# Performance work log

Hardware: AMD Instinct MI355X
Metric: run time of the kernel (lower is better)

The kernel has to match this reference:

```python
import jax, jax.numpy as jnp
import numpy as np

DT = 0.01
REG = 0.01

def setup_inputs() -> dict:
    key = jax.random.key(0)
    k1, k2, k3, k4 = jax.random.split(key, 4)
    B, C_in, L = 16, 128, 4096
    C_out, KS = 256, 9
    return {
        "x": jax.random.normal(k1, (B, C_in, L), dtype=jnp.float32),
        "weight": jax.random.normal(k2, (C_out, C_in, KS), dtype=jnp.float32) * np.sqrt(2.0 / (C_out * KS)),
        "bias": jnp.zeros((C_out,), dtype=jnp.float32),
        "vel": jax.random.normal(k3, (C_in, KS), dtype=jnp.float32) * 0.1,
        "acc": jax.random.normal(k4, (C_in, KS), dtype=jnp.float32) * 0.01,
        "ks": 9,
        "stride": 1,
        "pad": 4,
    }

def reference(x, weight, bias, vel, acc, ks, stride, pad):
    # x: [B, C_in, L]
    if pad > 0:
        x = jnp.pad(x, ((0, 0), (0, 0), (pad, pad)), mode="edge")  # replicate pad
    L_pad = x.shape[2]
    L_out = (L_pad - ks) // stride + 1
    t_off = jnp.arange(ks, dtype=jnp.float32) * DT  # [ks]
    # unfold: gather sliding windows -> [B, C_in, L_out, ks]
    idx = jnp.arange(L_out)[:, None] * stride + jnp.arange(ks)[None, :]
    xu = x[:, :, idx]
    # per-tap physics offset: vel*t + 0.5*acc*t^2, shape [C_in, ks] broadcast
    offset = vel * t_off + 0.5 * acc * (t_off ** 2)  # [C_in, ks]
    xt = xu + offset[None, :, None, :]  # [B, C_in, L_out, ks]
    # GEMM: [B, L_out, C_in*ks] x [C_in*ks, C_out]
    out = jnp.einsum("bclk,ock->bol", xt, weight) + bias[None, :, None]
    phys = REG * (jnp.mean(vel ** 2) + jnp.mean(acc ** 2))
    return (out, phys)
```

## Files before the change

### kernel.cpp

```cpp
#include <hip/hip_runtime.h>
#include <hip/hip_bf16.h>

typedef unsigned short u16;
typedef __bf16 bf16x8 __attribute__((ext_vector_type(8)));
typedef float f32x4 __attribute__((ext_vector_type(4)));
typedef unsigned short ushort8 __attribute__((ext_vector_type(8)));

#define C_IN   128
#define C_OUT  256
#define BATCH  16
#define LEN    4096
#define KS     9
#define PAD    4
#define LPAD   (LEN + 2*PAD)
#define KTOT   (C_IN * KS)
#define NSTEP  36

#define XT_BLKS    1040
#define W4_BLKS    1152
#define EB_BLKS    256

__device__ inline u16 f2bf(float f) {
    __hip_bfloat16 h = __float2bfloat16(f);
    return __builtin_bit_cast(u16, h);
}

__device__ __forceinline__ void g2l16(const void* g, void* l) {
    __builtin_amdgcn_global_load_lds(
        (const __attribute__((address_space(1))) void*)g,
        (__attribute__((address_space(3))) void*)l, 16, 0, 0);
}

__global__ void prep_all(const float* __restrict__ x, const float* __restrict__ w,
                         const float* __restrict__ bias, const float* __restrict__ vel,
                         const float* __restrict__ acc_in,
                         u16* __restrict__ xt, u16* __restrict__ w4,
                         float* __restrict__ ebias, float* __restrict__ phys_out) {
    int bid = blockIdx.x;
    int t = threadIdx.x;
    if (bid < XT_BLKS) {
        int b    = bid / 65;
        int lblk = bid % 65;
        int lane = t & 63;
        int jb   = t >> 6;
        int lp   = lblk * 64 + lane;
        if (lp >= LPAD) return;
        int l = lp - PAD;
        l = l < 0 ? 0 : (l > LEN - 1 ? LEN - 1 : l);
        const float* xb = x + (size_t)b * C_IN * LEN + l;
        u16* row = xt + ((size_t)b * LPAD + lp) * C_IN;
        int key = lp & 15;
        #pragma unroll
        for (int jj = 0; jj < 4; ++jj) {
            int cblk = jb * 4 + jj;
            ushort8 v;
            #pragma unroll
            for (int e = 0; e < 8; ++e)
                v[e] = f2bf(xb[(size_t)(cblk * 8 + e) * LEN]);
            int jstore = cblk ^ key;
            *reinterpret_cast<ushort8*>(row + jstore * 8) = v;
        }
        return;
    }
    if (bid < XT_BLKS + W4_BLKS) {
        int i = (bid - XT_BLKS) * 256 + t;
        int e  = i & 7;
        int r  = i >> 3;
        int mr = r & 15;
        int kg = (r >> 4) & 3;
        int ob = (r >> 6) & 15;
        int s  = r >> 10;
        int o  = ob * 16 + mr;
        int k  = s >> 2;
        int c  = (s & 3) * 32 + kg * 8 + e;
        w4[i] = f2bf(w[((size_t)o * C_IN + c) * KS + k]);
        return;
    }
    __shared__ float red[256];
    int o = bid - (XT_BLKS + W4_BLKS);
    float sum = 0.f;
    for (int i = t; i < KTOT; i += 256) {
        int k = i % KS;
        float tk = k * 0.01f;
        float off = vel[i] * tk + 0.5f * acc_in[i] * tk * tk;
        sum += off * w[(size_t)o * KTOT + i];
    }
    red[t] = sum;
    __syncthreads();
    for (int h = 128; h > 0; h >>= 1) {
        if (t < h) red[t] += red[t + h];
        __syncthreads();
    }
    if (t == 0) ebias[o] = bias[o] + red[0];

    if (o == 0) {
        __syncthreads();
        float pv = 0.f;
        for (int i = t; i < KTOT; i += 256) {
            float v = vel[i], a = acc_in[i];
            pv += v * v + a * a;
        }
        red[t] = pv;
        __syncthreads();
        for (int h = 128; h > 0; h >>= 1) {
            if (t < h) red[t] += red[t + h];
            __syncthreads();
        }
        if (t == 0) *phys_out = 0.01f * (red[0] / (float)KTOT);
    }
}

__global__ __launch_bounds__(256, 2) void conv_main(const u16* __restrict__ xt,
                                                    const u16* __restrict__ w4,
                                                    const float* __restrict__ ebias,
                                                    float* __restrict__ out) {
    __shared__ u16 ldsx[17408];
    __shared__ u16 ldsa[2][8192];

    int b     = blockIdx.y;
    int lbase = blockIdx.x * 128;
    int t     = threadIdx.x;
    int lane  = t & 63;
    int w     = t >> 6;
    int wm    = w >> 1;
    int wn    = w & 1;
    int mrow  = lane & 15;
    int kgrp  = lane >> 4;

    {
        const u16* bsrc = xt + ((size_t)b * LPAD + lbase) * C_IN;
        #pragma unroll
        for (int j = 0; j < 8; ++j)
            g2l16(bsrc + (j * 256 + t) * 8, ldsx + (j * 256 + w * 64) * 8);
        if (t < 128)
            g2l16(bsrc + (2048 + t) * 8, ldsx + (2048 + w * 64) * 8);
        #pragma unroll
        for (int j = 0; j < 4; ++j)
            g2l16(w4 + (j * 256 + t) * 8, ldsa[0] + (j * 256 + w * 64) * 8);
    }
    __syncthreads();

    f32x4 acc[8][4] = {};
    const char* ldsbase = reinterpret_cast<const char*>(ldsx);
    int afoff = (wm << 13) + lane * 16;

    #define LOAD_A_BUF(BUF, AF)                                                  \
        {                                                                        \
            const char* ab_ = reinterpret_cast<const char*>(ldsa[BUF]) + afoff;  \
            _Pragma("unroll")                                                    \
            for (int mi = 0; mi < 8; ++mi)                                       \
                AF[mi] = *reinterpret_cast<const bf16x8*>(ab_ + (mi << 10));     \
        }
    #define LOAD_B(S, BF)                                                        \
        {                                                                        \
            int k_ = (S) >> 2;                                                   \
            int coff_ = ((S) & 3) * 64 + kgrp * 16;                              \
            _Pragma("unroll")                                                    \
            for (int ni = 0; ni < 4; ++ni) {                                     \
                int row_  = wn * 64 + ni * 16 + mrow + k_;                       \
                int addr_ = row_ * 256 + coff_;                                  \
                addr_ ^= (row_ & 15) << 4;                                       \
                BF[ni] = *reinterpret_cast<const bf16x8*>(ldsbase + addr_);      \
            }                                                                    \
        }
    #define STAGE_A(S, BUF)                                                      \
        {                                                                        \
            const u16* as_ = w4 + (size_t)(S) * 8192;                            \
            _Pragma("unroll")                                                    \
            for (int j = 0; j < 4; ++j)                                          \
                g2l16(as_ + (j * 256 + t) * 8, ldsa[BUF] + (j * 256 + w * 64) * 8); \
        }

    #pragma unroll
    for (int s = 0; s < NSTEP; ++s) {
        if (s + 1 < NSTEP) STAGE_A(s + 1, (s + 1) & 1);
        bf16x8 af[8], bf[4];
        LOAD_A_BUF(s & 1, af);
        LOAD_B(s, bf);
        #pragma unroll
        for (int mi = 0; mi < 8; ++mi)
            #pragma unroll
            for (int ni = 0; ni < 4; ++ni)
                acc[mi][ni] = __builtin_amdgcn_mfma_f32_16x16x32_bf16(
                    af[mi], bf[ni], acc[mi][ni], 0, 0, 0);
        if (s + 1 < NSTEP) {
            asm volatile("s_waitcnt vmcnt(0) lgkmcnt(0)" ::: "memory");
            __builtin_amdgcn_s_barrier();
        }
    }

    #pragma unroll
    for (int mi = 0; mi < 8; ++mi) {
        int o0 = wm * 128 + mi * 16 + kgrp * 4;
        f32x4 eb = *reinterpret_cast<const f32x4*>(ebias + o0);
        #pragma unroll
        for (int ni = 0; ni < 4; ++ni) {
            int l = lbase + wn * 64 + ni * 16 + mrow;
            float* op = out + (size_t)(b * C_OUT + o0) * LEN + l;
            #pragma unroll
            for (int r = 0; r < 4; ++r)
                op[(size_t)r * LEN] = acc[mi][ni][r] + eb[r];
        }
    }
    #undef LOAD_A_BUF
    #undef LOAD_B
    #undef STAGE_A
}

extern "C" void kernel_launch(void* const* d_in, const int* in_sizes, int n_in,
                              void* d_out, int out_size, void* d_ws, size_t ws_size,
                              hipStream_t stream) {
    const float* x      = (const float*)d_in[0];
    const float* weight = (const float*)d_in[1];
    const float* bias   = (const float*)d_in[2];
    const float* vel    = (const float*)d_in[3];
    const float* acc    = (const float*)d_in[4];
    float* out = (float*)d_out;

    char* ws = (char*)d_ws;
    u16*  xt    = (u16*)ws;
    u16*  w4    = (u16*)(ws + (size_t)BATCH * LPAD * C_IN * 2);
    float* ebias = (float*)(ws + (size_t)BATCH * LPAD * C_IN * 2 + (size_t)C_OUT * KTOT * 2);

    hipLaunchKernelGGL(prep_all, dim3(XT_BLKS + W4_BLKS + EB_BLKS), dim3(256), 0, stream,
                       x, weight, bias, vel, acc, xt, w4, ebias,
                       out + (size_t)BATCH * C_OUT * LEN);
    hipLaunchKernelGGL(conv_main, dim3(LEN / 128, BATCH), dim3(256), 0, stream,
                       xt, w4, ebias, out);
}
```

Measured before the change: 58.57 us.

## Load weight fragments directly from global into registers, drop LDS staging and barriers

The weight operand is no longer staged through double-buffered LDS with a block-wide barrier every step. Each wave now reads its own 64-row slice of weights straight from global memory into registers, with register double-buffering across steps. The warp tiling changes from a 2x2 grid to 4x1, so each wave covers all 128 positions and reads more B fragments from LDS. This removes per-step synchronisation and LDS traffic for A, at the cost of direct global latency being exposed and less A reuse across waves.

```diff
diff --git a/kernel.cpp b/kernel.cpp
--- a/kernel.cpp
+++ b/kernel.cpp
@@ -115,15 +115,13 @@
                                                     const float* __restrict__ ebias,
                                                     float* __restrict__ out) {
     __shared__ u16 ldsx[17408];
-    __shared__ u16 ldsa[2][8192];
 
     int b     = blockIdx.y;
     int lbase = blockIdx.x * 128;
     int t     = threadIdx.x;
     int lane  = t & 63;
     int w     = t >> 6;
-    int wm    = w >> 1;
-    int wn    = w & 1;
+    int wm    = w;
     int mrow  = lane & 15;
     int kgrp  = lane >> 4;
 
@@ -134,77 +132,66 @@
             g2l16(bsrc + (j * 256 + t) * 8, ldsx + (j * 256 + w * 64) * 8);
         if (t < 128)
             g2l16(bsrc + (2048 + t) * 8, ldsx + (2048 + w * 64) * 8);
-        #pragma unroll
-        for (int j = 0; j < 4; ++j)
-            g2l16(w4 + (j * 256 + t) * 8, ldsa[0] + (j * 256 + w * 64) * 8);
     }
     __syncthreads();
 
-    f32x4 acc[8][4] = {};
+    f32x4 acc[4][8] = {};
     const char* ldsbase = reinterpret_cast<const char*>(ldsx);
-    int afoff = (wm << 13) + lane * 16;
-
-    #define LOAD_A_BUF(BUF, AF)                                                  \
+    const u16* alane = w4 + ((size_t)(wm * 4) * 64 + lane) * 8;
+
+    #define LOAD_A(S, AF)                                                        \
         {                                                                        \
-            const char* ab_ = reinterpret_cast<const char*>(ldsa[BUF]) + afoff;  \
+            const u16* p_ = alane + (size_t)(S) * 8192;                          \
             _Pragma("unroll")                                                    \
-            for (int mi = 0; mi < 8; ++mi)                                       \
-                AF[mi] = *reinterpret_cast<const bf16x8*>(ab_ + (mi << 10));     \
-        }
-    #define LOAD_B(S, BF)                                                        \
+            for (int mi = 0; mi < 4; ++mi)                                       \
+                AF[mi] = *reinterpret_cast<const bf16x8*>(p_ + mi * 512);        \
+        }
+    #define STEP(S, AF)                                                          \
         {                                                                        \
             int k_ = (S) >> 2;                                                   \
             int coff_ = ((S) & 3) * 64 + kgrp * 16;                              \
+            bf16x8 bf_[8];                                                       \
             _Pragma("unroll")                                                    \
-            for (int ni = 0; ni < 4; ++ni) {                                     \
-                int row_  = wn * 64 + ni * 16 + mrow + k_;                       \
+            for (int ni = 0; ni < 8; ++ni) {                                     \
+                int row_  = ni * 16 + mrow + k_;                                 \
                 int addr_ = row_ * 256 + coff_;                                  \
                 addr_ ^= (row_ & 15) << 4;                                       \
-                BF[ni] = *reinterpret_cast<const bf16x8*>(ldsbase + addr_);      \
+                bf_[ni] = *reinterpret_cast<const bf16x8*>(ldsbase + addr_);     \
             }                                                                    \
-        }
-    #define STAGE_A(S, BUF)                                                      \
-        {                                                                        \
-            const u16* as_ = w4 + (size_t)(S) * 8192;                            \
             _Pragma("unroll")                                                    \
-            for (int j = 0; j < 4; ++j)                                          \
-                g2l16(as_ + (j * 256 + t) * 8, ldsa[BUF] + (j * 256 + w * 64) * 8); \
-        }
+            for (int mi = 0; mi < 4; ++mi)                                       \
+                _Pragma("unroll")                                                \
+                for (int ni = 0; ni < 8; ++ni)                                   \
+                    acc[mi][ni] = __builtin_amdgcn_mfma_f32_16x16x32_bf16(       \
+                        AF[mi], bf_[ni], acc[mi][ni], 0, 0, 0);                  \
+        }
+
+    bf16x8 afA[4], afB[4];
+    LOAD_A(0, afA);
 
     #pragma unroll
-    for (int s = 0; s < NSTEP; ++s) {
-        if (s + 1 < NSTEP) STAGE_A(s + 1, (s + 1) & 1);
-        bf16x8 af[8], bf[4];
-        LOAD_A_BUF(s & 1, af);
-        LOAD_B(s, bf);
-        #pragma unroll
-        for (int mi = 0; mi < 8; ++mi)
-            #pragma unroll
-            for (int ni = 0; ni < 4; ++ni)
-                acc[mi][ni] = __builtin_amdgcn_mfma_f32_16x16x32_bf16(
-                    af[mi], bf[ni], acc[mi][ni], 0, 0, 0);
-        if (s + 1 < NSTEP) {
-            asm volatile("s_waitcnt vmcnt(0) lgkmcnt(0)" ::: "memory");
-            __builtin_amdgcn_s_barrier();
-        }
+    for (int s = 0; s < NSTEP; s += 2) {
+        if (s + 1 < NSTEP) LOAD_A(s + 1, afB);
+        STEP(s, afA);
+        if (s + 2 < NSTEP) LOAD_A(s + 2, afA);
+        STEP(s + 1, afB);
     }
 
     #pragma unroll
-    for (int mi = 0; mi < 8; ++mi) {
-        int o0 = wm * 128 + mi * 16 + kgrp * 4;
+    for (int mi = 0; mi < 4; ++mi) {
+        int o0 = wm * 64 + mi * 16 + kgrp * 4;
         f32x4 eb = *reinterpret_cast<const f32x4*>(ebias + o0);
         #pragma unroll
-        for (int ni = 0; ni < 4; ++ni) {
-            int l = lbase + wn * 64 + ni * 16 + mrow;
+        for (int ni = 0; ni < 8; ++ni) {
+            int l = lbase + ni * 16 + mrow;
             float* op = out + (size_t)(b * C_OUT + o0) * LEN + l;
             #pragma unroll
             for (int r = 0; r < 4; ++r)
                 op[(size_t)r * LEN] = acc[mi][ni][r] + eb[r];
         }
     }
-    #undef LOAD_A_BUF
-    #undef LOAD_B
-    #undef STAGE_A
+    #undef LOAD_A
+    #undef STEP
 }
 
 extern "C" void kernel_launch(void* const* d_in, const int* in_sizes, int n_in,
```

After: 71.83 us. +22.6%, slower.

## Enlarge conv tile to 512 threads with triple-buffered weight pipeline and split MFMA phases

Applied to the files above, without the earlier changes.

Doubles the per-block L tile to 256 with 8 waves arranged 2x4, so each weight stage in LDS is shared by more output columns. Weight staging moves from double to triple buffering with a prefetch distance of two, and partial vmcnt waits replace full drains. Each step is split into two half-MFMA phases with interleaved LDS loads, barriers and s_setprio. The aim is to hide global-to-LDS latency and raise weight reuse. In exchange, LDS per block grows (about 115 KB), which may cut occupancy, and the grid halves to 256 blocks.

```diff
diff --git a/kernel.cpp b/kernel.cpp
--- a/kernel.cpp
+++ b/kernel.cpp
@@ -110,20 +110,20 @@
     }
 }
 
-__global__ __launch_bounds__(256, 2) void conv_main(const u16* __restrict__ xt,
+__global__ __launch_bounds__(512, 2) void conv_main(const u16* __restrict__ xt,
                                                     const u16* __restrict__ w4,
                                                     const float* __restrict__ ebias,
                                                     float* __restrict__ out) {
-    __shared__ u16 ldsx[17408];
-    __shared__ u16 ldsa[2][8192];
+    __shared__ u16 ldsx[4224 * 8];
+    __shared__ u16 ldsa[3][8192];
 
     int b     = blockIdx.y;
-    int lbase = blockIdx.x * 128;
+    int lbase = blockIdx.x * 256;
     int t     = threadIdx.x;
     int lane  = t & 63;
     int w     = t >> 6;
-    int wm    = w >> 1;
-    int wn    = w & 1;
+    int wm    = w >> 2;
+    int wn    = w & 3;
     int mrow  = lane & 15;
     int kgrp  = lane >> 4;
 
@@ -131,27 +131,30 @@
         const u16* bsrc = xt + ((size_t)b * LPAD + lbase) * C_IN;
         #pragma unroll
         for (int j = 0; j < 8; ++j)
-            g2l16(bsrc + (j * 256 + t) * 8, ldsx + (j * 256 + w * 64) * 8);
+            g2l16(bsrc + (j * 512 + t) * 8, ldsx + (j * 512 + w * 64) * 8);
         if (t < 128)
-            g2l16(bsrc + (2048 + t) * 8, ldsx + (2048 + w * 64) * 8);
-        #pragma unroll
-        for (int j = 0; j < 4; ++j)
-            g2l16(w4 + (j * 256 + t) * 8, ldsa[0] + (j * 256 + w * 64) * 8);
-    }
-    __syncthreads();
+            g2l16(bsrc + (4096 + t) * 8, ldsx + (4096 + w * 64) * 8);
+        #pragma unroll
+        for (int p = 0; p < 2; ++p)
+            #pragma unroll
+            for (int j = 0; j < 2; ++j)
+                g2l16(w4 + (size_t)p * 8192 + (j * 512 + t) * 8,
+                      ldsa[p] + (j * 512 + w * 64) * 8);
+    }
+    asm volatile("s_waitcnt vmcnt(2)" ::: "memory");
+    __builtin_amdgcn_s_barrier();
 
     f32x4 acc[8][4] = {};
     const char* ldsbase = reinterpret_cast<const char*>(ldsx);
-    int afoff = (wm << 13) + lane * 16;
-
-    #define LOAD_A_BUF(BUF, AF)                                                  \
+
+    #define LOAD_A4(BUF, M0, AF)                                                 \
         {                                                                        \
-            const char* ab_ = reinterpret_cast<const char*>(ldsa[BUF]) + afoff;  \
+            const u16* ab_ = ldsa[BUF] + wm * 4096 + (M0) * 512 + lane * 8;      \
             _Pragma("unroll")                                                    \
-            for (int mi = 0; mi < 8; ++mi)                                       \
-                AF[mi] = *reinterpret_cast<const bf16x8*>(ab_ + (mi << 10));     \
-        }
-    #define LOAD_B(S, BF)                                                        \
+            for (int mi = 0; mi < 4; ++mi)                                       \
+                AF[mi] = *reinterpret_cast<const bf16x8*>(ab_ + mi * 512);       \
+        }
+    #define LOAD_B4(S, BF)                                                       \
         {                                                                        \
             int k_ = (S) >> 2;                                                   \
             int coff_ = ((S) & 3) * 64 + kgrp * 16;                              \
@@ -163,35 +166,49 @@
                 BF[ni] = *reinterpret_cast<const bf16x8*>(ldsbase + addr_);      \
             }                                                                    \
         }
-    #define STAGE_A(S, BUF)                                                      \
+    #define STAGE_J(S, J)                                                        \
+        g2l16(w4 + (size_t)(S) * 8192 + ((J) * 512 + t) * 8,                     \
+              ldsa[(S) % 3] + ((J) * 512 + w * 64) * 8);
+    #define MFMA16(AF, BF, M0)                                                   \
         {                                                                        \
-            const u16* as_ = w4 + (size_t)(S) * 8192;                            \
             _Pragma("unroll")                                                    \
-            for (int j = 0; j < 4; ++j)                                          \
-                g2l16(as_ + (j * 256 + t) * 8, ldsa[BUF] + (j * 256 + w * 64) * 8); \
+            for (int mi = 0; mi < 4; ++mi)                                       \
+                _Pragma("unroll")                                                \
+                for (int ni = 0; ni < 4; ++ni)                                   \
+                    acc[(M0) + mi][ni] = __builtin_amdgcn_mfma_f32_16x16x32_bf16(\
+                        AF[mi], BF[ni], acc[(M0) + mi][ni], 0, 0, 0);            \
         }
 
     #pragma unroll
     for (int s = 0; s < NSTEP; ++s) {
-        if (s + 1 < NSTEP) STAGE_A(s + 1, (s + 1) & 1);
-        bf16x8 af[8], bf[4];
-        LOAD_A_BUF(s & 1, af);
-        LOAD_B(s, bf);
-        #pragma unroll
-        for (int mi = 0; mi < 8; ++mi)
-            #pragma unroll
-            for (int ni = 0; ni < 4; ++ni)
-                acc[mi][ni] = __builtin_amdgcn_mfma_f32_16x16x32_bf16(
-                    af[mi], bf[ni], acc[mi][ni], 0, 0, 0);
-        if (s + 1 < NSTEP) {
-            asm volatile("s_waitcnt vmcnt(0) lgkmcnt(0)" ::: "memory");
-            __builtin_amdgcn_s_barrier();
-        }
+        const int buf = s % 3;
+        bf16x8 af[4], bf[4];
+        LOAD_A4(buf, 0, af);
+        LOAD_B4(s, bf);
+        if (s + 2 < NSTEP) STAGE_J(s + 2, 0)
+        __builtin_amdgcn_s_barrier();
+        asm volatile("s_waitcnt lgkmcnt(0)" ::: "memory");
+        __builtin_amdgcn_sched_barrier(0);
+        __builtin_amdgcn_s_setprio(1);
+        MFMA16(af, bf, 0);
+        __builtin_amdgcn_s_setprio(0);
+        __builtin_amdgcn_s_barrier();
+        LOAD_A4(buf, 4, af);
+        if (s + 2 < NSTEP) STAGE_J(s + 2, 1)
+        __builtin_amdgcn_s_barrier();
+        asm volatile("s_waitcnt lgkmcnt(0)" ::: "memory");
+        __builtin_amdgcn_sched_barrier(0);
+        __builtin_amdgcn_s_setprio(1);
+        MFMA16(af, bf, 4);
+        __builtin_amdgcn_s_setprio(0);
+        if (s + 2 < NSTEP)      asm volatile("s_waitcnt vmcnt(2)" ::: "memory");
+        else if (s + 1 < NSTEP) asm volatile("s_waitcnt vmcnt(0)" ::: "memory");
+        __builtin_amdgcn_s_barrier();
     }
 
     #pragma unroll
     for (int mi = 0; mi < 8; ++mi) {
-        int o0 = wm * 128 + mi * 16 + kgrp * 4;
+        int o0 = (wm * 8 + mi) * 16 + kgrp * 4;
         f32x4 eb = *reinterpret_cast<const f32x4*>(ebias + o0);
         #pragma unroll
         for (int ni = 0; ni < 4; ++ni) {
@@ -202,9 +219,10 @@
                 op[(size_t)r * LEN] = acc[mi][ni][r] + eb[r];
         }
     }
-    #undef LOAD_A_BUF
-    #undef LOAD_B
-    #undef STAGE_A
+    #undef LOAD_A4
+    #undef LOAD_B4
+    #undef STAGE_J
+    #undef MFMA16
 }
 
 extern "C" void kernel_launch(void* const* d_in, const int* in_sizes, int n_in,
@@ -225,6 +243,6 @@
     hipLaunchKernelGGL(prep_all, dim3(XT_BLKS + W4_BLKS + EB_BLKS), dim3(256), 0, stream,
                        x, weight, bias, vel, acc, xt, w4, ebias,
                        out + (size_t)BATCH * C_OUT * LEN);
-    hipLaunchKernelGGL(conv_main, dim3(LEN / 128, BATCH), dim3(256), 0, stream,
+    hipLaunchKernelGGL(conv_main, dim3(LEN / 256, BATCH), dim3(512), 0, stream,
                        xt, w4, ebias, out);
 }
```

Result: slower. 66.62 us (+13.7%).
